# Performance work log

Measured on AMD Instinct MI355X. Metric: run time of the kernel, lower is better.

The kernel has to match this reference:

```python
import jax, jax.numpy as jnp
import numpy as np

B, T = 2, 2048
D_MODEL, D_HIDDEN = 1024, 2048
N_EXPERTS, TOP_K = 8, 2
N_TOKENS = B * T
CAPACITY = 2 * N_TOKENS * TOP_K // N_EXPERTS  # 4096


def setup_inputs() -> dict:
    key = jax.random.key(0)
    k_x, k_rw, k_w, k_v, k_o = jax.random.split(key, 5)
    x = jax.random.normal(k_x, (B, T, D_MODEL), jnp.float32)
    # router: nn.Linear(d_model, n_experts) -> weight [E, D], bias [E]
    router_w = jax.random.normal(k_rw, (N_EXPERTS, D_MODEL), jnp.float32) * D_MODEL ** -0.5
    router_b = jnp.zeros((N_EXPERTS,), jnp.float32)
    # stacked expert params, matching SwiGLU init scales
    W = jax.random.normal(k_w, (N_EXPERTS, D_MODEL, D_HIDDEN), jnp.float32) * D_MODEL ** -0.5
    V = jax.random.normal(k_v, (N_EXPERTS, D_MODEL, D_HIDDEN), jnp.float32) * D_MODEL ** -0.5
    W_out = jax.random.normal(k_o, (N_EXPERTS, D_HIDDEN, D_MODEL), jnp.float32) * D_HIDDEN ** -0.5
    return {"x": x, "router_w": router_w, "router_b": router_b, "W": W, "V": V, "W_out": W_out}


def reference(x, router_w, router_b, W, V, W_out):
    Bq, Tq, D = x.shape
    N = Bq * Tq
    x_flat = x.reshape(N, D)

    # token-level top-k routing
    router_logits = x_flat @ router_w.T + router_b            # [N, E]
    top_vals, top_ids = jax.lax.top_k(router_logits, TOP_K)   # [N, K]
    top_probs = jax.nn.softmax(top_vals, axis=-1)             # [N, K]

    # pad row N: gathers with fill index N read zeros / contribute zero weight
    x_pad = jnp.concatenate([x_flat, jnp.zeros((1, D), x_flat.dtype)], axis=0)
    probs_pad = jnp.concatenate([top_probs, jnp.zeros((1, TOP_K), top_probs.dtype)], axis=0)

    out = jnp.zeros((N + 1, D), x_flat.dtype)
    for e in range(N_EXPERTS):  # static small loop over experts
        tok, slot = jnp.nonzero(top_ids == e, size=CAPACITY, fill_value=(N, 0))
        w = probs_pad[tok, slot][:, None]     # [C, 1], zero for padding slots
        xin = x_pad[tok]                      # [C, D] gather
        a = xin @ W[e]                        # [C, H]
        b = xin @ V[e]                        # [C, H]
        y = (a * (b * jax.nn.sigmoid(b))) @ W_out[e]  # SwiGLU: a * swish(b) -> [C, D]
        out = out.at[tok].add(y * w)          # weighted scatter-add
    return out[:N].reshape(Bq, Tq, D)
```

## Files before the change

### kernel.cpp

```cpp
#include <hip/hip_runtime.h>
#include <cstdint>
#include <cstddef>

#define N_TOK 4096
#define DM    1024
#define DH    2048
#define NE    8
#define NSLOT 8192

typedef short bf16x8_t __attribute__((ext_vector_type(8)));
typedef float f32x4    __attribute__((ext_vector_type(4)));
typedef unsigned short u16x8 __attribute__((ext_vector_type(8)));

__device__ __forceinline__ unsigned short f2bf(float f) {
  union { float f; unsigned int u; } v; v.f = f;
  unsigned int u = v.u;
  u += 0x7fffu + ((u >> 16) & 1u);
  return (unsigned short)(u >> 16);
}

__device__ __forceinline__ float bf2f(unsigned short h) {
  union { unsigned int u; float f; } v; v.u = ((unsigned int)h) << 16;
  return v.f;
}

#define GLD16(gp, lp)                                                          \
  __builtin_amdgcn_global_load_lds(                                            \
      (const __attribute__((address_space(1))) void*)(gp),                     \
      (__attribute__((address_space(3))) void*)(lp), 16, 0, 0)

__device__ __forceinline__ int expert_off(const int* __restrict__ counts, int e, int* cnt) {
  int off = 0, s = 0;
#pragma unroll
  for (int i = 0; i < NE; i++) { if (i == e) off = s; s += counts[i]; }
  *cnt = counts[e];
  return off;
}

__global__ __launch_bounds__(256) void k_transpose(
    const float* __restrict__ W, const float* __restrict__ V,
    const float* __restrict__ Wout, unsigned short* __restrict__ B1t,
    unsigned short* __restrict__ B2t, int* __restrict__ counts) {
  if (blockIdx.z == 0 && blockIdx.x == 0 && blockIdx.y == 0 && threadIdx.x < NE)
    counts[threadIdx.x] = 0;

  const int z = blockIdx.z;
  const float* s;
  unsigned short* d;
  int R, C, xt, yt;
  if (z < 16) {
    const int e = z & 7;
    s = ((z < 8) ? W : V) + (size_t)e * DM * DH;
    d = B1t + (size_t)e * 4096 * DM + (size_t)((z < 8) ? 0 : DH) * DM;
    R = DM; C = DH; xt = blockIdx.x; yt = blockIdx.y;
  } else {
    const int e = z - 16;
    s = Wout + (size_t)e * DH * DM;
    d = B2t + (size_t)e * DM * DH;
    R = DH; C = DM;
    const int flat = blockIdx.x * 16 + blockIdx.y;
    xt = flat & 15; yt = flat >> 4;
  }
  const int c0 = xt * 64, r0 = yt * 64;
  __shared__ float tile[64][65];
  const int t = threadIdx.x;
  {
    const int cc = (t & 15) * 4;
#pragma unroll
    for (int j = 0; j < 4; j++) {
      const int r = (t >> 4) + j * 16;
      const float4 v = *(const float4*)(s + (size_t)(r0 + r) * C + c0 + cc);
      tile[r][cc + 0] = v.x; tile[r][cc + 1] = v.y;
      tile[r][cc + 2] = v.z; tile[r][cc + 3] = v.w;
    }
  }
  __syncthreads();
  {
    const int r8 = (t & 7) * 8;
#pragma unroll
    for (int j = 0; j < 2; j++) {
      const int c = (t >> 3) + j * 32;
      u16x8 o;
#pragma unroll
      for (int i = 0; i < 8; i++) o[i] = f2bf(tile[r8 + i][c]);
      *(u16x8*)(d + (size_t)(c0 + c) * R + r0 + r8) = o;
    }
  }
}

__global__ __launch_bounds__(256) void k_router(
    const float* __restrict__ x, const float* __restrict__ rw,
    const float* __restrict__ rb, int* __restrict__ counts,
    int* __restrict__ meta_e, int* __restrict__ meta_idx,
    float* __restrict__ meta_p) {
  const int wv = threadIdx.x >> 6;
  const int l  = threadIdx.x & 63;
  const int tk = blockIdx.x * 4 + wv;
  const float* xr = x + (size_t)tk * DM;

  float acc[NE];
#pragma unroll
  for (int e = 0; e < NE; e++) acc[e] = 0.f;
#pragma unroll 4
  for (int i = 0; i < DM / 64; i++) {
    const float xv = xr[i * 64 + l];
#pragma unroll
    for (int e = 0; e < NE; e++) acc[e] += xv * rw[e * DM + i * 64 + l];
  }
#pragma unroll
  for (int off = 32; off > 0; off >>= 1) {
#pragma unroll
    for (int e = 0; e < NE; e++) acc[e] += __shfl_xor(acc[e], off);
  }
#pragma unroll
  for (int e = 0; e < NE; e++) acc[e] += rb[e];

  float v0 = -1e30f; int e0 = 0;
#pragma unroll
  for (int e = 0; e < NE; e++) { if (acc[e] > v0) { v0 = acc[e]; e0 = e; } }
  float v1 = -1e30f; int e1 = 0;
#pragma unroll
  for (int e = 0; e < NE; e++) { if (e != e0 && acc[e] > v1) { v1 = acc[e]; e1 = e; } }
  const float p0 = 1.0f / (1.0f + __expf(v1 - v0));
  const float p1 = 1.0f - p0;

  if (l == 0) {
    const int i0 = atomicAdd(&counts[e0], 1);
    const int i1 = atomicAdd(&counts[e1], 1);
    meta_e[tk * 2 + 0] = e0;  meta_e[tk * 2 + 1] = e1;
    meta_idx[tk * 2 + 0] = i0; meta_idx[tk * 2 + 1] = i1;
    meta_p[tk * 2 + 0] = p0;  meta_p[tk * 2 + 1] = p1;
  }
}

__global__ __launch_bounds__(256) void k_gather(
    const float* __restrict__ x, const int* __restrict__ meta_e,
    const int* __restrict__ meta_idx, const int* __restrict__ counts,
    unsigned short* __restrict__ Xg) {
  const int tk = blockIdx.x;
  int offs[NE];
  { int s = 0;
#pragma unroll
    for (int e = 0; e < NE; e++) { offs[e] = s; s += counts[e]; } }
  const int s0 = tk * 2, s1 = s0 + 1;
  const int g0 = offs[meta_e[s0]] + meta_idx[s0];
  const int g1 = offs[meta_e[s1]] + meta_idx[s1];
  const float4 v = ((const float4*)(x + (size_t)tk * DM))[threadIdx.x];
  ushort4 o;
  o.x = f2bf(v.x); o.y = f2bf(v.y); o.z = f2bf(v.z); o.w = f2bf(v.w);
  *(ushort4*)(Xg + (size_t)g0 * DM + threadIdx.x * 4) = o;
  *(ushort4*)(Xg + (size_t)g1 * DM + threadIdx.x * 4) = o;
}

__global__ __launch_bounds__(256, 2) void k_gemm1(
    const unsigned short* __restrict__ Xg, const unsigned short* __restrict__ B1t,
    unsigned short* __restrict__ G, const int* __restrict__ counts) {
  const int e = blockIdx.z;
  int cnt;
  const int off = expert_off(counts, e, &cnt);
  const int mt = blockIdx.y;
  if (mt * 128 >= cnt) return;
  const int h0 = blockIdx.x * 128;
  const int row_base = off + mt * 128;

  __shared__ unsigned short As[2][128 * 32];
  __shared__ unsigned short Ws[2][128 * 32];
  __shared__ unsigned short Vs[2][128 * 32];

  const int t = threadIdx.x;
  const int l = t & 63;
  const int w = t >> 6;
  const int wm = (w >> 1) * 64;
  const int wn = (w & 1) * 64;
  const int lr = l & 15;
  const int kq = (l >> 4) * 8;

  const unsigned short* Bw = B1t + ((size_t)e * 4096 + h0) * DM;
  const unsigned short* Bv = Bw + (size_t)DH * DM;

  const int c0 = t, c1 = t + 256;
  const int ar0 = c0 >> 2, ak0 = (c0 & 3) * 8;
  const int ar1 = c1 >> 2, ak1 = (c1 & 3) * 8;
  const int arow0 = min(row_base + ar0, NSLOT - 1);
  const int arow1 = min(row_base + ar1, NSLOT - 1);

  f32x4 acc_a[4][4], acc_b[4][4];
  const f32x4 z4 = {0.f, 0.f, 0.f, 0.f};
#pragma unroll
  for (int i = 0; i < 4; i++)
#pragma unroll
    for (int j = 0; j < 4; j++) { acc_a[i][j] = z4; acc_b[i][j] = z4; }

  for (int k0 = 0; k0 < DM; k0 += 64) {
    __syncthreads();
    GLD16(Xg + (size_t)arow0 * DM + k0 + ak0,      &As[0][c0 * 8]);
    GLD16(Xg + (size_t)arow1 * DM + k0 + ak1,      &As[0][c1 * 8]);
    GLD16(Xg + (size_t)arow0 * DM + k0 + 32 + ak0, &As[1][c0 * 8]);
    GLD16(Xg + (size_t)arow1 * DM + k0 + 32 + ak1, &As[1][c1 * 8]);
    GLD16(Bw + (size_t)ar0 * DM + k0 + ak0,        &Ws[0][c0 * 8]);
    GLD16(Bw + (size_t)ar1 * DM + k0 + ak1,        &Ws[0][c1 * 8]);
    GLD16(Bw + (size_t)ar0 * DM + k0 + 32 + ak0,   &Ws[1][c0 * 8]);
    GLD16(Bw + (size_t)ar1 * DM + k0 + 32 + ak1,   &Ws[1][c1 * 8]);
    GLD16(Bv + (size_t)ar0 * DM + k0 + ak0,        &Vs[0][c0 * 8]);
    GLD16(Bv + (size_t)ar1 * DM + k0 + ak1,        &Vs[0][c1 * 8]);
    GLD16(Bv + (size_t)ar0 * DM + k0 + 32 + ak0,   &Vs[1][c0 * 8]);
    GLD16(Bv + (size_t)ar1 * DM + k0 + 32 + ak1,   &Vs[1][c1 * 8]);
    __syncthreads();

#pragma unroll
    for (int ks = 0; ks < 2; ks++) {
      bf16x8_t af[4], wf[4], vf[4];
#pragma unroll
      for (int mi = 0; mi < 4; mi++)
        af[mi] = *(const bf16x8_t*)&As[ks][(wm + mi * 16 + lr) * 32 + kq];
#pragma unroll
      for (int ni = 0; ni < 4; ni++) {
        wf[ni] = *(const bf16x8_t*)&Ws[ks][(wn + ni * 16 + lr) * 32 + kq];
        vf[ni] = *(const bf16x8_t*)&Vs[ks][(wn + ni * 16 + lr) * 32 + kq];
      }
#pragma unroll
      for (int mi = 0; mi < 4; mi++)
#pragma unroll
        for (int ni = 0; ni < 4; ni++) {
          acc_a[mi][ni] = __builtin_amdgcn_mfma_f32_16x16x32_bf16(af[mi], wf[ni], acc_a[mi][ni], 0, 0, 0);
          acc_b[mi][ni] = __builtin_amdgcn_mfma_f32_16x16x32_bf16(af[mi], vf[ni], acc_b[mi][ni], 0, 0, 0);
        }
    }
  }

  const int q4 = (l >> 4) * 4;
#pragma unroll
  for (int mi = 0; mi < 4; mi++) {
#pragma unroll
    for (int r = 0; r < 4; r++) {
      const int mloc = mt * 128 + wm + mi * 16 + q4 + r;
      if (mloc >= cnt) continue;
      unsigned short* grow = G + (size_t)(off + mloc) * DH;
#pragma unroll
      for (int ni = 0; ni < 4; ni++) {
        const int h = h0 + wn + ni * 16 + lr;
        const float a = acc_a[mi][ni][r];
        const float b = acc_b[mi][ni][r];
        const float s = b / (1.0f + __expf(-b));
        grow[h] = f2bf(a * s);
      }
    }
  }
}

__global__ __launch_bounds__(256, 2) void k_gemm2(
    const unsigned short* __restrict__ G, const unsigned short* __restrict__ B2t,
    unsigned short* __restrict__ Y, const int* __restrict__ counts) {
  const int z = blockIdx.z;
  const int e = z & 7;
  const int half = z >> 3;
  int cnt;
  const int off = expert_off(counts, e, &cnt);
  const int mt = blockIdx.y;
  if (mt * 128 >= cnt) return;
  const int n0 = blockIdx.x * 128;
  const int row_base = off + mt * 128;
  const int kbase = half * 1024;

  __shared__ unsigned short As[2][128 * 32];
  __shared__ unsigned short Bs[2][128 * 32];

  const int t = threadIdx.x;
  const int l = t & 63;
  const int w = t >> 6;
  const int wm = (w >> 1) * 64;
  const int wn = (w & 1) * 64;
  const int lr = l & 15;
  const int kq = (l >> 4) * 8;

  const unsigned short* Bp = B2t + ((size_t)e * DM + n0) * DH;

  const int c0 = t, c1 = t + 256;
  const int ar0 = c0 >> 2, ak0 = (c0 & 3) * 8;
  const int ar1 = c1 >> 2, ak1 = (c1 & 3) * 8;
  const int arow0 = min(row_base + ar0, NSLOT - 1);
  const int arow1 = min(row_base + ar1, NSLOT - 1);

  f32x4 acc[4][4];
  const f32x4 z4 = {0.f, 0.f, 0.f, 0.f};
#pragma unroll
  for (int i = 0; i < 4; i++)
#pragma unroll
    for (int j = 0; j < 4; j++) acc[i][j] = z4;

  for (int kk = 0; kk < 1024; kk += 64) {
    const int k0 = kbase + kk;
    __syncthreads();
    GLD16(G + (size_t)arow0 * DH + k0 + ak0,      &As[0][c0 * 8]);
    GLD16(G + (size_t)arow1 * DH + k0 + ak1,      &As[0][c1 * 8]);
    GLD16(G + (size_t)arow0 * DH + k0 + 32 + ak0, &As[1][c0 * 8]);
    GLD16(G + (size_t)arow1 * DH + k0 + 32 + ak1, &As[1][c1 * 8]);
    GLD16(Bp + (size_t)ar0 * DH + k0 + ak0,       &Bs[0][c0 * 8]);
    GLD16(Bp + (size_t)ar1 * DH + k0 + ak1,       &Bs[0][c1 * 8]);
    GLD16(Bp + (size_t)ar0 * DH + k0 + 32 + ak0,  &Bs[1][c0 * 8]);
    GLD16(Bp + (size_t)ar1 * DH + k0 + 32 + ak1,  &Bs[1][c1 * 8]);
    __syncthreads();

#pragma unroll
    for (int ks = 0; ks < 2; ks++) {
      bf16x8_t af[4], bf[4];
#pragma unroll
      for (int mi = 0; mi < 4; mi++)
        af[mi] = *(const bf16x8_t*)&As[ks][(wm + mi * 16 + lr) * 32 + kq];
#pragma unroll
      for (int ni = 0; ni < 4; ni++)
        bf[ni] = *(const bf16x8_t*)&Bs[ks][(wn + ni * 16 + lr) * 32 + kq];
#pragma unroll
      for (int mi = 0; mi < 4; mi++)
#pragma unroll
        for (int ni = 0; ni < 4; ni++)
          acc[mi][ni] = __builtin_amdgcn_mfma_f32_16x16x32_bf16(af[mi], bf[ni], acc[mi][ni], 0, 0, 0);
    }
  }

  unsigned short* Yh = Y + (size_t)half * NSLOT * DM;
  const int q4 = (l >> 4) * 4;
#pragma unroll
  for (int mi = 0; mi < 4; mi++) {
#pragma unroll
    for (int r = 0; r < 4; r++) {
      const int mloc = mt * 128 + wm + mi * 16 + q4 + r;
      if (mloc >= cnt) continue;
      unsigned short* yrow = Yh + (size_t)(off + mloc) * DM;
#pragma unroll
      for (int ni = 0; ni < 4; ni++)
        yrow[n0 + wn + ni * 16 + lr] = f2bf(acc[mi][ni][r]);
    }
  }
}

__global__ __launch_bounds__(256) void k_combine(
    const unsigned short* __restrict__ Y, const int* __restrict__ meta_e,
    const int* __restrict__ meta_idx, const float* __restrict__ meta_p,
    const int* __restrict__ counts, float* __restrict__ out) {
  const int tk = blockIdx.x;
  int offs[NE];
  { int s = 0;
#pragma unroll
    for (int e = 0; e < NE; e++) { offs[e] = s; s += counts[e]; } }
  const int s0 = tk * 2, s1 = s0 + 1;
  const int g0 = offs[meta_e[s0]] + meta_idx[s0];
  const int g1 = offs[meta_e[s1]] + meta_idx[s1];
  const float w0 = meta_p[s0], w1 = meta_p[s1];
  const unsigned short* Y1 = Y + (size_t)NSLOT * DM;
  const ushort4 a0 = ((const ushort4*)(Y  + (size_t)g0 * DM))[threadIdx.x];
  const ushort4 a1 = ((const ushort4*)(Y1 + (size_t)g0 * DM))[threadIdx.x];
  const ushort4 b0 = ((const ushort4*)(Y  + (size_t)g1 * DM))[threadIdx.x];
  const ushort4 b1 = ((const ushort4*)(Y1 + (size_t)g1 * DM))[threadIdx.x];
  float4 o;
  o.x = w0 * (bf2f(a0.x) + bf2f(a1.x)) + w1 * (bf2f(b0.x) + bf2f(b1.x));
  o.y = w0 * (bf2f(a0.y) + bf2f(a1.y)) + w1 * (bf2f(b0.y) + bf2f(b1.y));
  o.z = w0 * (bf2f(a0.z) + bf2f(a1.z)) + w1 * (bf2f(b0.z) + bf2f(b1.z));
  o.w = w0 * (bf2f(a0.w) + bf2f(a1.w)) + w1 * (bf2f(b0.w) + bf2f(b1.w));
  ((float4*)(out + (size_t)tk * DM))[threadIdx.x] = o;
}

extern "C" void kernel_launch(void* const* d_in, const int* in_sizes, int n_in,
                              void* d_out, int out_size, void* d_ws, size_t ws_size,
                              hipStream_t stream) {
  const float* x    = (const float*)d_in[0];
  const float* rw   = (const float*)d_in[1];
  const float* rb   = (const float*)d_in[2];
  const float* W    = (const float*)d_in[3];
  const float* V    = (const float*)d_in[4];
  const float* Wout = (const float*)d_in[5];
  float* out = (float*)d_out;

  char* p = (char*)d_ws;
  unsigned short* B1t = (unsigned short*)p; p += (size_t)NE * 4096 * DM * 2;
  unsigned short* Y   = (unsigned short*)B1t;
  unsigned short* B2t = (unsigned short*)p; p += (size_t)NE * DM * DH * 2;
  unsigned short* Xg  = (unsigned short*)p; p += (size_t)NSLOT * DM * 2;
  unsigned short* G   = (unsigned short*)p; p += (size_t)NSLOT * DH * 2;
  int*   counts      = (int*)p;   p += 256;
  int*   meta_e      = (int*)p;   p += (size_t)N_TOK * 2 * 4;
  int*   meta_idx    = (int*)p;   p += (size_t)N_TOK * 2 * 4;
  float* meta_p      = (float*)p; p += (size_t)N_TOK * 2 * 4;

  k_transpose<<<dim3(32, 16, 24), 256, 0, stream>>>(W, V, Wout, B1t, B2t, counts);
  k_router<<<N_TOK / 4, 256, 0, stream>>>(x, rw, rb, counts, meta_e, meta_idx, meta_p);
  k_gather<<<N_TOK, 256, 0, stream>>>(x, meta_e, meta_idx, counts, Xg);
  k_gemm1<<<dim3(DH / 128, NSLOT / 128, NE), 256, 0, stream>>>(Xg, B1t, G, counts);
  k_gemm2<<<dim3(DM / 128, NSLOT / 128, 2 * NE), 256, 0, stream>>>(G, B2t, Y, counts);
  k_combine<<<N_TOK, 256, 0, stream>>>(Y, meta_e, meta_idx, meta_p, counts, out);
}
```

Baseline: 492.9 us.

## Shrink GEMM N-tiles to 64, drop gemm2 split-K, raise occupancy

```diff
diff --git a/kernel.cpp b/kernel.cpp
--- a/kernel.cpp
+++ b/kernel.cpp
@@ -152,7 +152,7 @@
   *(ushort4*)(Xg + (size_t)g1 * DM + threadIdx.x * 4) = o;
 }
 
-__global__ __launch_bounds__(256, 2) void k_gemm1(
+__global__ __launch_bounds__(256, 3) void k_gemm1(
     const unsigned short* __restrict__ Xg, const unsigned short* __restrict__ B1t,
     unsigned short* __restrict__ G, const int* __restrict__ counts) {
   const int e = blockIdx.z;
@@ -160,68 +160,63 @@
   const int off = expert_off(counts, e, &cnt);
   const int mt = blockIdx.y;
   if (mt * 128 >= cnt) return;
-  const int h0 = blockIdx.x * 128;
+  const int h0 = blockIdx.x * 64;
   const int row_base = off + mt * 128;
 
   __shared__ unsigned short As[2][128 * 32];
-  __shared__ unsigned short Ws[2][128 * 32];
-  __shared__ unsigned short Vs[2][128 * 32];
+  __shared__ unsigned short Ws[2][64 * 32];
+  __shared__ unsigned short Vs[2][64 * 32];
 
   const int t = threadIdx.x;
   const int l = t & 63;
   const int w = t >> 6;
-  const int wm = (w >> 1) * 64;
-  const int wn = (w & 1) * 64;
+  const int wm = (w & 1) * 64;
+  const int wn = (w >> 1) * 32;
   const int lr = l & 15;
   const int kq = (l >> 4) * 8;
 
   const unsigned short* Bw = B1t + ((size_t)e * 4096 + h0) * DM;
   const unsigned short* Bv = Bw + (size_t)DH * DM;
 
-  const int c0 = t, c1 = t + 256;
-  const int ar0 = c0 >> 2, ak0 = (c0 & 3) * 8;
-  const int ar1 = c1 >> 2, ak1 = (c1 & 3) * 8;
+  const int ar0 = t >> 2, ak0 = (t & 3) * 8;
   const int arow0 = min(row_base + ar0, NSLOT - 1);
-  const int arow1 = min(row_base + ar1, NSLOT - 1);
-
-  f32x4 acc_a[4][4], acc_b[4][4];
+  const int arow1 = min(row_base + ar0 + 64, NSLOT - 1);
+  const int br = t >> 2, bk = (t & 3) * 8;
+
+  f32x4 acc_a[4][2], acc_b[4][2];
   const f32x4 z4 = {0.f, 0.f, 0.f, 0.f};
 #pragma unroll
   for (int i = 0; i < 4; i++)
 #pragma unroll
-    for (int j = 0; j < 4; j++) { acc_a[i][j] = z4; acc_b[i][j] = z4; }
+    for (int j = 0; j < 2; j++) { acc_a[i][j] = z4; acc_b[i][j] = z4; }
 
   for (int k0 = 0; k0 < DM; k0 += 64) {
     __syncthreads();
-    GLD16(Xg + (size_t)arow0 * DM + k0 + ak0,      &As[0][c0 * 8]);
-    GLD16(Xg + (size_t)arow1 * DM + k0 + ak1,      &As[0][c1 * 8]);
-    GLD16(Xg + (size_t)arow0 * DM + k0 + 32 + ak0, &As[1][c0 * 8]);
-    GLD16(Xg + (size_t)arow1 * DM + k0 + 32 + ak1, &As[1][c1 * 8]);
-    GLD16(Bw + (size_t)ar0 * DM + k0 + ak0,        &Ws[0][c0 * 8]);
-    GLD16(Bw + (size_t)ar1 * DM + k0 + ak1,        &Ws[0][c1 * 8]);
-    GLD16(Bw + (size_t)ar0 * DM + k0 + 32 + ak0,   &Ws[1][c0 * 8]);
-    GLD16(Bw + (size_t)ar1 * DM + k0 + 32 + ak1,   &Ws[1][c1 * 8]);
-    GLD16(Bv + (size_t)ar0 * DM + k0 + ak0,        &Vs[0][c0 * 8]);
-    GLD16(Bv + (size_t)ar1 * DM + k0 + ak1,        &Vs[0][c1 * 8]);
-    GLD16(Bv + (size_t)ar0 * DM + k0 + 32 + ak0,   &Vs[1][c0 * 8]);
-    GLD16(Bv + (size_t)ar1 * DM + k0 + 32 + ak1,   &Vs[1][c1 * 8]);
+    GLD16(Xg + (size_t)arow0 * DM + k0 + ak0,      &As[0][t * 8]);
+    GLD16(Xg + (size_t)arow1 * DM + k0 + ak0,      &As[0][(t + 256) * 8]);
+    GLD16(Xg + (size_t)arow0 * DM + k0 + 32 + ak0, &As[1][t * 8]);
+    GLD16(Xg + (size_t)arow1 * DM + k0 + 32 + ak0, &As[1][(t + 256) * 8]);
+    GLD16(Bw + (size_t)br * DM + k0 + bk,          &Ws[0][t * 8]);
+    GLD16(Bw + (size_t)br * DM + k0 + 32 + bk,     &Ws[1][t * 8]);
+    GLD16(Bv + (size_t)br * DM + k0 + bk,          &Vs[0][t * 8]);
+    GLD16(Bv + (size_t)br * DM + k0 + 32 + bk,     &Vs[1][t * 8]);
     __syncthreads();
 
 #pragma unroll
     for (int ks = 0; ks < 2; ks++) {
-      bf16x8_t af[4], wf[4], vf[4];
+      bf16x8_t af[4], wf[2], vf[2];
 #pragma unroll
       for (int mi = 0; mi < 4; mi++)
         af[mi] = *(const bf16x8_t*)&As[ks][(wm + mi * 16 + lr) * 32 + kq];
 #pragma unroll
-      for (int ni = 0; ni < 4; ni++) {
+      for (int ni = 0; ni < 2; ni++) {
         wf[ni] = *(const bf16x8_t*)&Ws[ks][(wn + ni * 16 + lr) * 32 + kq];
         vf[ni] = *(const bf16x8_t*)&Vs[ks][(wn + ni * 16 + lr) * 32 + kq];
       }
 #pragma unroll
       for (int mi = 0; mi < 4; mi++)
 #pragma unroll
-        for (int ni = 0; ni < 4; ni++) {
+        for (int ni = 0; ni < 2; ni++) {
           acc_a[mi][ni] = __builtin_amdgcn_mfma_f32_16x16x32_bf16(af[mi], wf[ni], acc_a[mi][ni], 0, 0, 0);
           acc_b[mi][ni] = __builtin_amdgcn_mfma_f32_16x16x32_bf16(af[mi], vf[ni], acc_b[mi][ni], 0, 0, 0);
         }
@@ -237,7 +232,7 @@
       if (mloc >= cnt) continue;
       unsigned short* grow = G + (size_t)(off + mloc) * DH;
 #pragma unroll
-      for (int ni = 0; ni < 4; ni++) {
+      for (int ni = 0; ni < 2; ni++) {
         const int h = h0 + wn + ni * 16 + lr;
         const float a = acc_a[mi][ni][r];
         const float b = acc_b[mi][ni][r];
@@ -248,77 +243,69 @@
   }
 }
 
-__global__ __launch_bounds__(256, 2) void k_gemm2(
+__global__ __launch_bounds__(256, 3) void k_gemm2(
     const unsigned short* __restrict__ G, const unsigned short* __restrict__ B2t,
     unsigned short* __restrict__ Y, const int* __restrict__ counts) {
-  const int z = blockIdx.z;
-  const int e = z & 7;
-  const int half = z >> 3;
+  const int e = blockIdx.z;
   int cnt;
   const int off = expert_off(counts, e, &cnt);
   const int mt = blockIdx.y;
   if (mt * 128 >= cnt) return;
-  const int n0 = blockIdx.x * 128;
+  const int n0 = blockIdx.x * 64;
   const int row_base = off + mt * 128;
-  const int kbase = half * 1024;
 
   __shared__ unsigned short As[2][128 * 32];
-  __shared__ unsigned short Bs[2][128 * 32];
+  __shared__ unsigned short Bs[2][64 * 32];
 
   const int t = threadIdx.x;
   const int l = t & 63;
   const int w = t >> 6;
-  const int wm = (w >> 1) * 64;
-  const int wn = (w & 1) * 64;
+  const int wm = (w & 1) * 64;
+  const int wn = (w >> 1) * 32;
   const int lr = l & 15;
   const int kq = (l >> 4) * 8;
 
   const unsigned short* Bp = B2t + ((size_t)e * DM + n0) * DH;
 
-  const int c0 = t, c1 = t + 256;
-  const int ar0 = c0 >> 2, ak0 = (c0 & 3) * 8;
-  const int ar1 = c1 >> 2, ak1 = (c1 & 3) * 8;
+  const int ar0 = t >> 2, ak0 = (t & 3) * 8;
   const int arow0 = min(row_base + ar0, NSLOT - 1);
-  const int arow1 = min(row_base + ar1, NSLOT - 1);
-
-  f32x4 acc[4][4];
+  const int arow1 = min(row_base + ar0 + 64, NSLOT - 1);
+  const int br = t >> 2, bk = (t & 3) * 8;
+
+  f32x4 acc[4][2];
   const f32x4 z4 = {0.f, 0.f, 0.f, 0.f};
 #pragma unroll
   for (int i = 0; i < 4; i++)
 #pragma unroll
-    for (int j = 0; j < 4; j++) acc[i][j] = z4;
-
-  for (int kk = 0; kk < 1024; kk += 64) {
-    const int k0 = kbase + kk;
+    for (int j = 0; j < 2; j++) acc[i][j] = z4;
+
+  for (int k0 = 0; k0 < DH; k0 += 64) {
     __syncthreads();
-    GLD16(G + (size_t)arow0 * DH + k0 + ak0,      &As[0][c0 * 8]);
-    GLD16(G + (size_t)arow1 * DH + k0 + ak1,      &As[0][c1 * 8]);
-    GLD16(G + (size_t)arow0 * DH + k0 + 32 + ak0, &As[1][c0 * 8]);
-    GLD16(G + (size_t)arow1 * DH + k0 + 32 + ak1, &As[1][c1 * 8]);
-    GLD16(Bp + (size_t)ar0 * DH + k0 + ak0,       &Bs[0][c0 * 8]);
-    GLD16(Bp + (size_t)ar1 * DH + k0 + ak1,       &Bs[0][c1 * 8]);
-    GLD16(Bp + (size_t)ar0 * DH + k0 + 32 + ak0,  &Bs[1][c0 * 8]);
-    GLD16(Bp + (size_t)ar1 * DH + k0 + 32 + ak1,  &Bs[1][c1 * 8]);
+    GLD16(G + (size_t)arow0 * DH + k0 + ak0,      &As[0][t * 8]);
+    GLD16(G + (size_t)arow1 * DH + k0 + ak0,      &As[0][(t + 256) * 8]);
+    GLD16(G + (size_t)arow0 * DH + k0 + 32 + ak0, &As[1][t * 8]);
+    GLD16(G + (size_t)arow1 * DH + k0 + 32 + ak0, &As[1][(t + 256) * 8]);
+    GLD16(Bp + (size_t)br * DH + k0 + bk,         &Bs[0][t * 8]);
+    GLD16(Bp + (size_t)br * DH + k0 + 32 + bk,    &Bs[1][t * 8]);
     __syncthreads();
 
 #pragma unroll
     for (int ks = 0; ks < 2; ks++) {
-      bf16x8_t af[4], bf[4];
+      bf16x8_t af[4], bf[2];
 #pragma unroll
       for (int mi = 0; mi < 4; mi++)
         af[mi] = *(const bf16x8_t*)&As[ks][(wm + mi * 16 + lr) * 32 + kq];
 #pragma unroll
-      for (int ni = 0; ni < 4; ni++)
+      for (int ni = 0; ni < 2; ni++)
         bf[ni] = *(const bf16x8_t*)&Bs[ks][(wn + ni * 16 + lr) * 32 + kq];
 #pragma unroll
       for (int mi = 0; mi < 4; mi++)
 #pragma unroll
-        for (int ni = 0; ni < 4; ni++)
+        for (int ni = 0; ni < 2; ni++)
           acc[mi][ni] = __builtin_amdgcn_mfma_f32_16x16x32_bf16(af[mi], bf[ni], acc[mi][ni], 0, 0, 0);
     }
   }
 
-  unsigned short* Yh = Y + (size_t)half * NSLOT * DM;
   const int q4 = (l >> 4) * 4;
 #pragma unroll
   for (int mi = 0; mi < 4; mi++) {
@@ -326,9 +313,9 @@
     for (int r = 0; r < 4; r++) {
       const int mloc = mt * 128 + wm + mi * 16 + q4 + r;
       if (mloc >= cnt) continue;
-      unsigned short* yrow = Yh + (size_t)(off + mloc) * DM;
-#pragma unroll
-      for (int ni = 0; ni < 4; ni++)
+      unsigned short* yrow = Y + (size_t)(off + mloc) * DM;
+#pragma unroll
+      for (int ni = 0; ni < 2; ni++)
         yrow[n0 + wn + ni * 16 + lr] = f2bf(acc[mi][ni][r]);
     }
   }
@@ -347,16 +334,13 @@
   const int g0 = offs[meta_e[s0]] + meta_idx[s0];
   const int g1 = offs[meta_e[s1]] + meta_idx[s1];
   const float w0 = meta_p[s0], w1 = meta_p[s1];
-  const unsigned short* Y1 = Y + (size_t)NSLOT * DM;
-  const ushort4 a0 = ((const ushort4*)(Y  + (size_t)g0 * DM))[threadIdx.x];
-  const ushort4 a1 = ((const ushort4*)(Y1 + (size_t)g0 * DM))[threadIdx.x];
-  const ushort4 b0 = ((const ushort4*)(Y  + (size_t)g1 * DM))[threadIdx.x];
-  const ushort4 b1 = ((const ushort4*)(Y1 + (size_t)g1 * DM))[threadIdx.x];
+  const ushort4 a = ((const ushort4*)(Y + (size_t)g0 * DM))[threadIdx.x];
+  const ushort4 b = ((const ushort4*)(Y + (size_t)g1 * DM))[threadIdx.x];
   float4 o;
-  o.x = w0 * (bf2f(a0.x) + bf2f(a1.x)) + w1 * (bf2f(b0.x) + bf2f(b1.x));
-  o.y = w0 * (bf2f(a0.y) + bf2f(a1.y)) + w1 * (bf2f(b0.y) + bf2f(b1.y));
-  o.z = w0 * (bf2f(a0.z) + bf2f(a1.z)) + w1 * (bf2f(b0.z) + bf2f(b1.z));
-  o.w = w0 * (bf2f(a0.w) + bf2f(a1.w)) + w1 * (bf2f(b0.w) + bf2f(b1.w));
+  o.x = w0 * bf2f(a.x) + w1 * bf2f(b.x);
+  o.y = w0 * bf2f(a.y) + w1 * bf2f(b.y);
+  o.z = w0 * bf2f(a.z) + w1 * bf2f(b.z);
+  o.w = w0 * bf2f(a.w) + w1 * bf2f(b.w);
   ((float4*)(out + (size_t)tk * DM))[threadIdx.x] = o;
 }
 
@@ -385,7 +369,7 @@
   k_transpose<<<dim3(32, 16, 24), 256, 0, stream>>>(W, V, Wout, B1t, B2t, counts);
   k_router<<<N_TOK / 4, 256, 0, stream>>>(x, rw, rb, counts, meta_e, meta_idx, meta_p);
   k_gather<<<N_TOK, 256, 0, stream>>>(x, meta_e, meta_idx, counts, Xg);
-  k_gemm1<<<dim3(DH / 128, NSLOT / 128, NE), 256, 0, stream>>>(Xg, B1t, G, counts);
-  k_gemm2<<<dim3(DM / 128, NSLOT / 128, 2 * NE), 256, 0, stream>>>(G, B2t, Y, counts);
+  k_gemm1<<<dim3(DH / 64, NSLOT / 128, NE), 256, 0, stream>>>(Xg, B1t, G, counts);
+  k_gemm2<<<dim3(DM / 64, NSLOT / 128, NE), 256, 0, stream>>>(G, B2t, Y, counts);
   k_combine<<<N_TOK, 256, 0, stream>>>(Y, meta_e, meta_idx, meta_p, counts, out);
 }
```

Measured after the change: 503.3 us. 2.1% more time.
